# Kernel optimization log

Hardware: AMD Instinct MI355X
Metric: run time of the kernel (lower is better)

## Reference

```python
import jax, jax.numpy as jnp
import numpy as np

EPS = 1e-20
BETA = 0.25


def setup_inputs() -> dict:
    key = jax.random.key(0)
    k1, k2, k3 = jax.random.split(key, 3)
    B, N, D = 8192, 8192, 512
    x = jax.random.normal(k1, (B, D), dtype=jnp.float32)
    codebook = jax.random.normal(k2, (N, D), dtype=jnp.float32)
    u = jax.random.uniform(k3, (B, N), dtype=jnp.float32)
    return {"x": x, "codebook": codebook, "u": u}


def reference(x, codebook, u):
    # gumbel noise from uniform samples (matches sample_gumble)
    g = -jnp.log(-jnp.log(u + EPS) + EPS)  # [B, N]
    dist = (jnp.sum(x * x, axis=1, keepdims=True)
            - 2.0 * (x @ codebook.T)
            + jnp.sum(codebook * codebook, axis=1)[None, :])
    # topk(k=1) over -dist == argmin over dist
    ind = jnp.argmin(dist, axis=1)  # [B]
    # gumbel_softmax with temperature=1.0 on logits=-dist
    weights = jax.nn.softmax(-dist + g, axis=-1)  # [B, N]
    quantized = weights @ codebook  # [B, D]
    sg = jax.lax.stop_gradient
    loss = (BETA * jnp.sum((x - sg(quantized)) ** 2, axis=-1)
            + jnp.sum((sg(x) - quantized) ** 2, axis=-1))  # [B]
    return quantized, ind, loss
```

## Files before the change

kernel.cpp:

```cpp
#include <hip/hip_runtime.h>
#include <math.h>

constexpr int B = 8192, N = 8192, D = 512;
constexpr float EPSF = 1e-20f;
constexpr float SKIP   = 20.0f;
constexpr float GMAX   = 17.0f;
constexpr float DELTAF = 1.0f;
constexpr float DELTA  = 0.05f;
constexpr int CAP  = 96;
constexpr int DCAP = 48;

typedef short bf16x8 __attribute__((ext_vector_type(8)));
typedef float f32x4 __attribute__((ext_vector_type(4)));

__device__ inline unsigned short f2bf(float f) {
    unsigned x = __float_as_uint(f);
    unsigned r = x + 0x7FFFu + ((x >> 16) & 1u);
    return (unsigned short)(r >> 16);
}
__device__ inline float bf2f(unsigned short h) {
    return __uint_as_float(((unsigned)h) << 16);
}
__device__ inline unsigned fmap(float f) {
    unsigned b = __float_as_uint(f);
    return b ^ ((unsigned)((int)b >> 31) | 0x80000000u);
}
__device__ inline float funmap(unsigned u) {
    unsigned b = u ^ ((~(unsigned)((int)u >> 31)) | 0x80000000u);
    return __uint_as_float(b);
}
__device__ inline void gload16(const void* g, void* l) {
    __builtin_amdgcn_global_load_lds(
        (const __attribute__((address_space(1))) void*)g,
        (__attribute__((address_space(3))) void*)l, 16, 0, 0);
}


__global__ __launch_bounds__(256) void vq_prep(const float* __restrict__ x,
        const float* __restrict__ cb, unsigned short* __restrict__ ch,
        float* __restrict__ cnorm, float* __restrict__ xnorm,
        int* __restrict__ counts, int* __restrict__ dcounts) {
    int w = threadIdx.x >> 6, lane = threadIdx.x & 63;
    int gid = blockIdx.x * 256 + threadIdx.x;
    if (gid < 2 * B) { counts[gid] = 0; dcounts[gid] = 0; }
    int v = blockIdx.x * 4 + w;
    if (v < N) {
        const float4* s4 = reinterpret_cast<const float4*>(cb + (size_t)v * D) + lane * 2;
        float4 a = s4[0], c = s4[1];
        float vals[8] = {a.x, a.y, a.z, a.w, c.x, c.y, c.z, c.w};
        float ns = 0.f;
        unsigned short hb[8];
        #pragma unroll
        for (int e = 0; e < 8; ++e) {
            float vv = vals[e];
            ns += vv * vv;
            hb[e] = f2bf(vv);
        }
        #pragma unroll
        for (int off = 1; off < 64; off <<= 1) ns += __shfl_xor(ns, off);
        if (lane == 0) cnorm[v] = ns;
        *reinterpret_cast<bf16x8*>(ch + (size_t)v * D + lane * 8) = *reinterpret_cast<bf16x8*>(hb);
    } else {
        int b = v - N;
        const float4* s4 = reinterpret_cast<const float4*>(x + (size_t)b * D) + lane * 2;
        float4 a = s4[0], c = s4[1];
        float ns = a.x*a.x + a.y*a.y + a.z*a.z + a.w*a.w
                 + c.x*c.x + c.y*c.y + c.z*c.z + c.w*c.w;
        #pragma unroll
        for (int off = 1; off < 64; off <<= 1) ns += __shfl_xor(ns, off);
        if (lane == 0) xnorm[b] = ns;
    }
}

constexpr int OFF_B0 = 0;
constexpr int OFF_RM = 65536;
constexpr int OFF_R1 = 65792;
constexpr int OFF_CT = 66048;
constexpr int OFF_DC = 66304;
constexpr int OFF_P1 = 66560;
constexpr int OFF_P2 = 67072;
constexpr int OFF_PI = 67584;
constexpr int SMEM_BYTES = 68096;

__global__ __launch_bounds__(512, 2) void vq_mfma(
        const float* __restrict__ x, const unsigned short* __restrict__ ch,
        const float* __restrict__ cnorm, const float* __restrict__ xnorm,
        const float* __restrict__ u,
        int2* __restrict__ lists, int* __restrict__ counts,
        int* __restrict__ dlists, int* __restrict__ dcounts,
        float* __restrict__ m1h, float* __restrict__ m2h, int* __restrict__ i1h) {

    __shared__ __align__(16) unsigned char smem[SMEM_BYTES];

    const int tid = threadIdx.x, w = tid >> 6, lane = tid & 63;
    const int wm = w >> 1, wn = w & 1, l15 = lane & 15, g = lane >> 4;
    const int rg = blockIdx.x >> 1, half = blockIdx.x & 1;
    const int rbase = rg * 64, nb0 = half * 4096;

    bf16x8 ah[16];
    {
        const float* xp = x + (size_t)(rbase + wm * 16 + l15) * D + g * 8;
        #pragma unroll
        for (int ks = 0; ks < 16; ++ks) {
            const float4* p = reinterpret_cast<const float4*>(xp + ks * 32);
            float4 v0 = p[0], v1 = p[1];
            float vv[8] = {v0.x, v0.y, v0.z, v0.w, v1.x, v1.y, v1.z, v1.w};
            unsigned short hh[8];
            #pragma unroll
            for (int e = 0; e < 8; ++e) hh[e] = f2bf(vv[e]);
            ah[ks] = *reinterpret_cast<bf16x8*>(hh);
        }
    }
    float xn_r[4];
    #pragma unroll
    for (int r = 0; r < 4; ++r) xn_r[r] = xnorm[rbase + wm * 16 + g * 4 + r];

    if (tid < 64) {
        *(unsigned*)(smem + OFF_RM + tid * 4) = fmap(-INFINITY);
        *(unsigned*)(smem + OFF_R1 + tid * 4) = fmap(INFINITY);
        *(int*)(smem + OFF_CT + tid * 4) = 0;
        *(int*)(smem + OFF_DC + tid * 4) = 0;
    }

    float d1[4], d2[4], lmax[4]; int i1[4];
    #pragma unroll
    for (int r = 0; r < 4; ++r) {
        d1[r] = INFINITY; d2[r] = INFINITY; lmax[r] = -INFINITY; i1[r] = 0;
    }

    auto stage = [&](int nbn) {
        #pragma unroll
        for (int j = 0; j < 8; ++j) {
            const int row = w * 8 + j;
            const int c = (lane ^ j) * 8;
            gload16(ch + (size_t)(nbn + row) * D + c,
                    smem + OFF_B0 + row * 1024);
        }
    };

    stage(nb0);
    __syncthreads();

    const int colA = wn * 32 + l15;
    const int xr = colA & 7;
    const unsigned char* baseH = smem + OFF_B0 + colA * 1024;
    const float* ubase = u + (size_t)(rbase + wm * 16 + g * 4) * N + wn * 32 + l15;

    float dsv_prev[2][4], ur_prev[2][4];

    auto epi_fast = [&](float (&dsvX)[2][4], float (&urX)[2][4], int nbX) {
        float rmF[4], r1F[4];
        #pragma unroll
        for (int r = 0; r < 4; ++r) {
            int rl = wm * 16 + g * 4 + r;
            rmF[r] = funmap(*(const unsigned*)(smem + OFF_RM + rl * 4));
            r1F[r] = funmap(*(const unsigned*)(smem + OFF_R1 + rl * 4));
        }
        #pragma unroll
        for (int f = 0; f < 2; ++f)
            #pragma unroll
            for (int r = 0; r < 4; ++r) {
                const int rl = wm * 16 + g * 4 + r;
                const int grow = rbase + rl;
                float ds = dsvX[f][r];
                int cidx = nbX + wn * 32 + f * 16 + l15;
                if (ds < d1[r]) { d2[r] = d1[r]; d1[r] = ds; i1[r] = cidx; }
                else if (ds < d2[r]) d2[r] = ds;
                bool need = (ds < fminf(r1F[r], d1[r]) + DELTAF)
                         || (ds < GMAX + SKIP - fmaxf(rmF[r], lmax[r]));
                if (__any(need)) {
                    float gn = -__logf(-__logf(urX[f][r] + EPSF) + EPSF);
                    float lg = gn - ds;
                    lmax[r] = fmaxf(lmax[r], lg);
                    if (ds < fminf(r1F[r], d1[r]) + DELTAF) {
                        int slot = atomicAdd((int*)(smem + OFF_DC + rl * 4), 1);
                        if (slot < DCAP) dlists[(size_t)(half * B + grow) * DCAP + slot] = cidx;
                    }
                    if (ds < r1F[r]) atomicMin((unsigned*)(smem + OFF_R1 + rl * 4), fmap(ds));
                    if (lg > fmaxf(rmF[r], lmax[r]) - SKIP) {
                        int slot = atomicAdd((int*)(smem + OFF_CT + rl * 4), 1);
                        if (slot < CAP)
                            lists[(size_t)(half * B + grow) * CAP + slot] =
                                make_int2(__float_as_int(lg), cidx);
                    }
                    if (lg > rmF[r]) atomicMax((unsigned*)(smem + OFF_RM + rl * 4), fmap(lg));
                }
            }
    };

    #pragma unroll 1
    for (int t = 0; t < 64; ++t) {
        const int nb = nb0 + t * 64;
        float ur[2][4];
        #pragma unroll
        for (int f = 0; f < 2; ++f)
            #pragma unroll
            for (int r = 0; r < 4; ++r)
                ur[f][r] = ubase[(size_t)r * N + f * 16 + nb];
        float cn0 = cnorm[nb + wn * 32 + l15];
        float cn1 = cnorm[nb + wn * 32 + 16 + l15];

        f32x4 a0e = {0.f,0.f,0.f,0.f}, a0o = {0.f,0.f,0.f,0.f};
        f32x4 a1e = {0.f,0.f,0.f,0.f}, a1o = {0.f,0.f,0.f,0.f};
        #pragma unroll
        for (int ks = 0; ks < 16; ++ks) {
            const int pos = (((ks * 4 + g) ^ xr) << 4);
            bf16x8 b0 = *reinterpret_cast<const bf16x8*>(baseH + pos);
            bf16x8 b1 = *reinterpret_cast<const bf16x8*>(baseH + 16 * 1024 + pos);
            if (ks & 1) {
                a0o = __builtin_amdgcn_mfma_f32_16x16x32_bf16(ah[ks], b0, a0o, 0, 0, 0);
                a1o = __builtin_amdgcn_mfma_f32_16x16x32_bf16(ah[ks], b1, a1o, 0, 0, 0);
            } else {
                a0e = __builtin_amdgcn_mfma_f32_16x16x32_bf16(ah[ks], b0, a0e, 0, 0, 0);
                a1e = __builtin_amdgcn_mfma_f32_16x16x32_bf16(ah[ks], b1, a1e, 0, 0, 0);
            }
        }
        __syncthreads();

        if (t < 63) stage(nb + 64);

        if (t >= 2) epi_fast(dsv_prev, ur_prev, nb - 64);

        float dsv[2][4];
        #pragma unroll
        for (int f = 0; f < 2; ++f)
            #pragma unroll
            for (int r = 0; r < 4; ++r) {
                float S = f ? (a1e[r] + a1o[r]) : (a0e[r] + a0o[r]);
                dsv[f][r] = xn_r[r] - 2.f * S + (f ? cn1 : cn0);
            }

        if (t == 0) {
            float lgv0[2][4];
            #pragma unroll
            for (int f = 0; f < 2; ++f)
                #pragma unroll
                for (int r = 0; r < 4; ++r) {
                    float ds = dsv[f][r];
                    float gn = -__logf(-__logf(ur[f][r] + EPSF) + EPSF);
                    lgv0[f][r] = gn - ds;
                    int cidx = nb + wn * 32 + f * 16 + l15;
                    if (ds < d1[r]) { d2[r] = d1[r]; d1[r] = ds; i1[r] = cidx; }
                    else if (ds < d2[r]) d2[r] = ds;
                    lmax[r] = fmaxf(lmax[r], lgv0[f][r]);
                }
            #pragma unroll
            for (int r = 0; r < 4; ++r) {
                float mx = lmax[r], mn = d1[r];
                #pragma unroll
                for (int off = 1; off < 16; off <<= 1) {
                    mx = fmaxf(mx, __shfl_xor(mx, off));
                    mn = fminf(mn, __shfl_xor(mn, off));
                }
                if (l15 == 0) {
                    int rl = wm * 16 + g * 4 + r;
                    atomicMax((unsigned*)(smem + OFF_RM + rl * 4), fmap(mx));
                    atomicMin((unsigned*)(smem + OFF_R1 + rl * 4), fmap(mn));
                }
            }
            __syncthreads();
            float rmF[4], r1F[4];
            #pragma unroll
            for (int r = 0; r < 4; ++r) {
                int rl = wm * 16 + g * 4 + r;
                rmF[r] = funmap(*(const unsigned*)(smem + OFF_RM + rl * 4));
                r1F[r] = funmap(*(const unsigned*)(smem + OFF_R1 + rl * 4));
            }
            #pragma unroll
            for (int f = 0; f < 2; ++f)
                #pragma unroll
                for (int r = 0; r < 4; ++r) {
                    const int rl = wm * 16 + g * 4 + r;
                    const int grow = rbase + rl;
                    float ds = dsv[f][r], lg = lgv0[f][r];
                    int cidx = nb + wn * 32 + f * 16 + l15;
                    if (ds < fminf(r1F[r], d1[r]) + DELTAF) {
                        int slot = atomicAdd((int*)(smem + OFF_DC + rl * 4), 1);
                        if (slot < DCAP) dlists[(size_t)(half * B + grow) * DCAP + slot] = cidx;
                    }
                    if (ds < r1F[r]) atomicMin((unsigned*)(smem + OFF_R1 + rl * 4), fmap(ds));
                    if (lg > fmaxf(rmF[r], lmax[r]) - SKIP) {
                        int slot = atomicAdd((int*)(smem + OFF_CT + rl * 4), 1);
                        if (slot < CAP)
                            lists[(size_t)(half * B + grow) * CAP + slot] =
                                make_int2(__float_as_int(lg), cidx);
                    }
                    if (lg > rmF[r]) atomicMax((unsigned*)(smem + OFF_RM + rl * 4), fmap(lg));
                }
        } else {
            #pragma unroll
            for (int f = 0; f < 2; ++f)
                #pragma unroll
                for (int r = 0; r < 4; ++r) {
                    dsv_prev[f][r] = dsv[f][r];
                    ur_prev[f][r] = ur[f][r];
                }
        }
        __syncthreads();
    }
    epi_fast(dsv_prev, ur_prev, nb0 + 63 * 64);

    #pragma unroll
    for (int r = 0; r < 4; ++r) {
        float D1 = d1[r], D2v = d2[r]; int I1 = i1[r];
        #pragma unroll
        for (int off = 1; off < 16; off <<= 1) {
            float o1 = __shfl_xor(D1, off), o2 = __shfl_xor(D2v, off);
            int oi = __shfl_xor(I1, off);
            if (o1 < D1 || (o1 == D1 && oi < I1)) { D2v = fminf(D1, o2); D1 = o1; I1 = oi; }
            else D2v = fminf(o1, D2v);
        }
        if (l15 == 0) {
            int rl = wm * 16 + g * 4 + r;
            *(float*)(smem + OFF_P1 + (wn * 64 + rl) * 4) = D1;
            *(float*)(smem + OFF_P2 + (wn * 64 + rl) * 4) = D2v;
            *(int*)(smem + OFF_PI + (wn * 64 + rl) * 4) = I1;
        }
    }
    __syncthreads();
    if (tid < 64) {
        float a1 = *(float*)(smem + OFF_P1 + tid * 4), a2 = *(float*)(smem + OFF_P2 + tid * 4);
        int ai = *(int*)(smem + OFF_PI + tid * 4);
        float b1 = *(float*)(smem + OFF_P1 + (64 + tid) * 4), b2 = *(float*)(smem + OFF_P2 + (64 + tid) * 4);
        int bi = *(int*)(smem + OFF_PI + (64 + tid) * 4);
        float m1, m2; int mi;
        if (b1 < a1 || (b1 == a1 && bi < ai)) { m1 = b1; mi = bi; m2 = fminf(a1, b2); }
        else                                  { m1 = a1; mi = ai; m2 = fminf(b1, a2); }
        int hrow = half * B + rbase + tid;
        m1h[hrow] = m1; m2h[hrow] = m2; i1h[hrow] = mi;
        counts[hrow] = *(int*)(smem + OFF_CT + tid * 4);
        dcounts[hrow] = *(int*)(smem + OFF_DC + tid * 4);
    }
}

__global__ __launch_bounds__(256) void vq_finalize(
        const float* __restrict__ cb, const float* __restrict__ x,
        const int2* __restrict__ lists, const int* __restrict__ counts,
        float* __restrict__ m1h, float* __restrict__ m2h, int* __restrict__ i1h,
        float* __restrict__ out_q, float* __restrict__ out_loss) {
    __shared__ int2 ebuf[4][2 * CAP];
    int w = threadIdx.x >> 6, lane = threadIdx.x & 63;
    int row = blockIdx.x * 4 + w;
    int n0 = counts[row];      if (n0 > CAP) n0 = CAP;
    int n1 = counts[B + row];  if (n1 > CAP) n1 = CAP;
    int n = n0 + n1;
    for (int e = lane; e < n0; e += 64) ebuf[w][e] = lists[(size_t)row * CAP + e];
    for (int e = lane; e < n1; e += 64) ebuf[w][n0 + e] = lists[(size_t)(B + row) * CAP + e];
    __syncthreads();
    float m = -INFINITY;
    for (int e = lane; e < n; e += 64) m = fmaxf(m, __int_as_float(ebuf[w][e].x));
    #pragma unroll
    for (int off = 1; off < 64; off <<= 1) m = fmaxf(m, __shfl_xor(m, off));
    float denom = 0.f;
    for (int e = lane; e < n; e += 64) denom += __expf(__int_as_float(ebuf[w][e].x) - m);
    #pragma unroll
    for (int off = 1; off < 64; off <<= 1) denom += __shfl_xor(denom, off);
    float q[8] = {0.f, 0.f, 0.f, 0.f, 0.f, 0.f, 0.f, 0.f};
    for (int e = 0; e < n; ++e) {
        int2 ent = ebuf[w][e];
        float wgt = __expf(__int_as_float(ent.x) - m);
        if (wgt < 1e-9f) continue;
        const float4* c4 = reinterpret_cast<const float4*>(cb + (size_t)ent.y * D + lane * 8);
        float4 c0 = c4[0], c1 = c4[1];
        q[0] += wgt * c0.x; q[1] += wgt * c0.y; q[2] += wgt * c0.z; q[3] += wgt * c0.w;
        q[4] += wgt * c1.x; q[5] += wgt * c1.y; q[6] += wgt * c1.z; q[7] += wgt * c1.w;
    }
    float inv = 1.f / denom;
    const float4* x4 = reinterpret_cast<const float4*>(x + (size_t)row * D + lane * 8);
    float4 xa = x4[0], xb = x4[1];
    float xs[8] = {xa.x, xa.y, xa.z, xa.w, xb.x, xb.y, xb.z, xb.w};
    float ls = 0.f;
    #pragma unroll
    for (int k = 0; k < 8; ++k) {
        q[k] *= inv;
        float dlt = xs[k] - q[k];
        ls += dlt * dlt;
    }
    float4 q0 = {q[0], q[1], q[2], q[3]}, q1 = {q[4], q[5], q[6], q[7]};
    float4* o = reinterpret_cast<float4*>(out_q + (size_t)row * D + lane * 8);
    o[0] = q0; o[1] = q1;
    #pragma unroll
    for (int off = 1; off < 64; off <<= 1) ls += __shfl_xor(ls, off);
    if (lane == 0) {
        out_loss[row] = 1.25f * ls;
        float a1 = m1h[row], a2 = m2h[row]; int ai = i1h[row];
        float b1 = m1h[B + row], b2 = m2h[B + row]; int bi = i1h[B + row];
        float mm1, mm2; int mi;
        if (b1 < a1 || (b1 == a1 && bi < ai)) { mm1 = b1; mi = bi; mm2 = fminf(a1, b2); }
        else                                  { mm1 = a1; mi = ai; mm2 = fminf(b1, a2); }
        m1h[row] = mm1; m2h[row] = mm2; i1h[row] = mi;
    }
}

__global__ __launch_bounds__(256) void vq_row_full(
        const float* __restrict__ x, const float* __restrict__ cb,
        const float* __restrict__ cnorm, const float* __restrict__ u,
        const int* __restrict__ counts,
        float* __restrict__ out_q, float* __restrict__ out_loss) {
    int row = blockIdx.x;
    if (counts[row] <= CAP && counts[B + row] <= CAP) return;
    int tid = threadIdx.x, wv_ = tid >> 6, lane = tid & 63;
    __shared__ float xs[D];
    __shared__ float red[4];
    __shared__ float wts[256]; __shared__ int ids[256]; __shared__ int nc;
    for (int i = tid; i < D; i += 256) xs[i] = x[(size_t)row * D + i];
    if (tid == 0) nc = 0;
    __syncthreads();
    float xn = 0.f;
    for (int i = tid; i < D; i += 256) xn += xs[i] * xs[i];
    #pragma unroll
    for (int off = 1; off < 64; off <<= 1) xn += __shfl_xor(xn, off);
    if (lane == 0) red[wv_] = xn;
    __syncthreads();
    xn = red[0] + red[1] + red[2] + red[3];
    __syncthreads();
    float m = -INFINITY;
    for (int n = tid; n < N; n += 256) {
        float dot = 0.f;
        const float* c = cb + (size_t)n * D;
        for (int d = 0; d < D; ++d) dot = fmaf(xs[d], c[d], dot);
        float lg = -__logf(-__logf(u[(size_t)row * N + n] + EPSF) + EPSF)
                 - (xn - 2.f * dot + cnorm[n]);
        m = fmaxf(m, lg);
    }
    #pragma unroll
    for (int off = 1; off < 64; off <<= 1) m = fmaxf(m, __shfl_xor(m, off));
    if (lane == 0) red[wv_] = m;
    __syncthreads();
    m = fmaxf(fmaxf(red[0], red[1]), fmaxf(red[2], red[3]));
    __syncthreads();
    float denom = 0.f;
    for (int n = tid; n < N; n += 256) {
        float dot = 0.f;
        const float* c = cb + (size_t)n * D;
        for (int d = 0; d < D; ++d) dot = fmaf(xs[d], c[d], dot);
        float lg = -__logf(-__logf(u[(size_t)row * N + n] + EPSF) + EPSF)
                 - (xn - 2.f * dot + cnorm[n]);
        float wv2 = __expf(lg - m);
        denom += wv2;
        if (wv2 > 1e-8f) {
            int s = atomicAdd(&nc, 1);
            if (s < 256) { wts[s] = wv2; ids[s] = n; }
        }
    }
    #pragma unroll
    for (int off = 1; off < 64; off <<= 1) denom += __shfl_xor(denom, off);
    if (lane == 0) red[wv_] = denom;
    __syncthreads();
    denom = red[0] + red[1] + red[2] + red[3];
    int ncl = nc < 256 ? nc : 256;
    float q0 = 0.f, q1 = 0.f;
    for (int e = 0; e < ncl; ++e) {
        const float* c = cb + (size_t)ids[e] * D;
        q0 += wts[e] * c[tid * 2];
        q1 += wts[e] * c[tid * 2 + 1];
    }
    q0 /= denom; q1 /= denom;
    out_q[(size_t)row * D + tid * 2] = q0;
    out_q[(size_t)row * D + tid * 2 + 1] = q1;
    float dl0 = xs[tid * 2] - q0, dl1 = xs[tid * 2 + 1] - q1;
    float ls = dl0 * dl0 + dl1 * dl1;
    #pragma unroll
    for (int off = 1; off < 64; off <<= 1) ls += __shfl_xor(ls, off);
    __syncthreads();
    if (lane == 0) red[wv_] = ls;
    __syncthreads();
    if (tid == 0) out_loss[row] = 1.25f * (red[0] + red[1] + red[2] + red[3]);
}

__global__ __launch_bounds__(256) void argmin_fix2(
        const float* __restrict__ x, const float* __restrict__ cb,
        const float* __restrict__ m1h, const float* __restrict__ m2h,
        const int* __restrict__ i1h,
        const int* __restrict__ dcounts, const int* __restrict__ dlists,
        float* __restrict__ out_ind) {
    int w = threadIdx.x >> 6, lane = threadIdx.x & 63;
    int row = blockIdx.x * 4 + w;
    if (m2h[row] - m1h[row] >= DELTAF) {
        if (lane == 0) out_ind[row] = (float)i1h[row];
        return;
    }
    const float4* x4 = reinterpret_cast<const float4*>(x + (size_t)row * D) + lane * 2;
    float4 xa = x4[0], xb = x4[1];
    double xd[8] = {(double)xa.x, (double)xa.y, (double)xa.z, (double)xa.w,
                    (double)xb.x, (double)xb.y, (double)xb.z, (double)xb.w};
    double bestv = 1e300; int besti = 0x7fffffff;

    auto evalCode = [&](int n) {
        const float4* c4 = reinterpret_cast<const float4*>(cb + (size_t)n * D) + lane * 2;
        float4 ca = c4[0], cbv = c4[1];
        double cd[8] = {(double)ca.x, (double)ca.y, (double)ca.z, (double)ca.w,
                        (double)cbv.x, (double)cbv.y, (double)cbv.z, (double)cbv.w};
        double s = 0.0;
        #pragma unroll
        for (int k = 0; k < 8; ++k) {
            double dlt = xd[k] - cd[k];
            s = fma(dlt, dlt, s);
        }
        #pragma unroll
        for (int off = 1; off < 64; off <<= 1) s += __shfl_xor(s, off);
        if (s < bestv || (s == bestv && n < besti)) { bestv = s; besti = n; }
    };

    int n0 = dcounts[row], n1 = dcounts[B + row];
    if (n0 <= DCAP && n1 <= DCAP) {
        evalCode(i1h[row]);
        for (int e = 0; e < n0; ++e) evalCode(dlists[(size_t)row * DCAP + e]);
        for (int e = 0; e < n1; ++e) evalCode(dlists[(size_t)(B + row) * DCAP + e]);
    } else {
        for (int n = 0; n < N; ++n) evalCode(n);
    }
    if (lane == 0) out_ind[row] = (float)besti;
}

constexpr int ROWS = 16;
constexpr int NT   = 256;
constexpr int DT   = 16;

__global__ __launch_bounds__(256) void prep_norms(const float* __restrict__ x,
                                                  const float* __restrict__ cb,
                                                  float* __restrict__ cnorm,
                                                  float* __restrict__ xnorm) {
    int wave = threadIdx.x >> 6, lane = threadIdx.x & 63;
    int v = blockIdx.x * 4 + wave;
    const float* src;
    float* dst;
    if (v < N) { src = cb + (size_t)v * D; dst = cnorm + v; }
    else       { int b = v - N; if (b >= B) return; src = x + (size_t)b * D; dst = xnorm + b; }
    const float4* s4 = reinterpret_cast<const float4*>(src) + lane * 2;
    float4 a = s4[0], c = s4[1];
    float s = a.x*a.x + a.y*a.y + a.z*a.z + a.w*a.w
            + c.x*c.x + c.y*c.y + c.z*c.z + c.w*c.w;
    #pragma unroll
    for (int off = 1; off < 64; off <<= 1) s += __shfl_xor(s, off);
    if (lane == 0) *dst = s;
}

__global__ __launch_bounds__(256) void vq_main(const float* __restrict__ x,
        const float* __restrict__ cb, const float* __restrict__ u,
        const float* __restrict__ cnorm, const float* __restrict__ xnorm,
        float* __restrict__ out_q, float* __restrict__ out_loss,
        float* __restrict__ m1w, float* __restrict__ m2w, int* __restrict__ i1w) {

    __shared__ float xs[ROWS][D];
    __shared__ float ct[DT][NT];

    const int tid  = threadIdx.x;
    const int wave = tid >> 6, lane = tid & 63;
    const int rbase = blockIdx.x * ROWS;
    const int wrow  = rbase + wave * 4;

    for (int i = tid; i < ROWS * (D / 4); i += 256)
        reinterpret_cast<float4*>(xs)[i] =
            reinterpret_cast<const float4*>(x + (size_t)rbase * D)[i];
    __syncthreads();

    float xn[4];
    #pragma unroll
    for (int r = 0; r < 4; ++r) xn[r] = xnorm[wrow + r];

    float m[4], denom[4], acc[4][8];
    float am1[4], am2[4]; int ai1[4];
    #pragma unroll
    for (int r = 0; r < 4; ++r) {
        m[r] = -INFINITY; denom[r] = 0.f;
        am1[r] = INFINITY; am2[r] = INFINITY; ai1[r] = 0;
        #pragma unroll
        for (int k = 0; k < 8; ++k) acc[r][k] = 0.f;
    }

    for (int nb = 0; nb < N; nb += NT) {
        float S[4][4];
        #pragma unroll
        for (int r = 0; r < 4; ++r)
            #pragma unroll
            for (int j = 0; j < 4; ++j) S[r][j] = 0.f;

        for (int db = 0; db < D; db += DT) {
            __syncthreads();
            {
                const float4* src = reinterpret_cast<const float4*>(
                        cb + (size_t)(nb + tid) * D + db);
                float4 a0 = src[0], a1 = src[1], a2 = src[2], a3 = src[3];
                ct[ 0][tid]=a0.x; ct[ 1][tid]=a0.y; ct[ 2][tid]=a0.z; ct[ 3][tid]=a0.w;
                ct[ 4][tid]=a1.x; ct[ 5][tid]=a1.y; ct[ 6][tid]=a1.z; ct[ 7][tid]=a1.w;
                ct[ 8][tid]=a2.x; ct[ 9][tid]=a2.y; ct[10][tid]=a2.z; ct[11][tid]=a2.w;
                ct[12][tid]=a3.x; ct[13][tid]=a3.y; ct[14][tid]=a3.z; ct[15][tid]=a3.w;
            }
            __syncthreads();
            #pragma unroll
            for (int dq = 0; dq < DT / 4; ++dq) {
                float creg[4][4];
                #pragma unroll
                for (int k = 0; k < 4; ++k) {
                    float4 cv = *reinterpret_cast<const float4*>(&ct[dq*4 + k][4*lane]);
                    creg[k][0]=cv.x; creg[k][1]=cv.y; creg[k][2]=cv.z; creg[k][3]=cv.w;
                }
                #pragma unroll
                for (int r = 0; r < 4; ++r) {
                    float4 xv = *reinterpret_cast<const float4*>(&xs[wave*4 + r][db + dq*4]);
                    float xr[4] = {xv.x, xv.y, xv.z, xv.w};
                    #pragma unroll
                    for (int k = 0; k < 4; ++k)
                        #pragma unroll
                        for (int j = 0; j < 4; ++j)
                            S[r][j] = fmaf(xr[k], creg[k][j], S[r][j]);
                }
            }
        }

        float4 cn4 = *reinterpret_cast<const float4*>(&cnorm[nb + 4*lane]);
        float cn[4] = {cn4.x, cn4.y, cn4.z, cn4.w};

        float logit[4][4], dist[4][4];
        #pragma unroll
        for (int r = 0; r < 4; ++r) {
            float4 u4 = *reinterpret_cast<const float4*>(
                    &u[(size_t)(wrow + r) * N + nb + 4*lane]);
            float uu[4] = {u4.x, u4.y, u4.z, u4.w};
            #pragma unroll
            for (int j = 0; j < 4; ++j) {
                float ds = xn[r] - 2.f * S[r][j] + cn[j];
                float gg  = -logf(-logf(uu[j] + EPSF) + EPSF);
                dist[r][j]  = ds;
                logit[r][j] = gg - ds;
            }
        }

        #pragma unroll
        for (int r = 0; r < 4; ++r) {
            float l1 = INFINITY, l2 = INFINITY; int li = 0;
            #pragma unroll
            for (int j = 0; j < 4; ++j) {
                float dv = dist[r][j]; int idx = nb + 4*lane + j;
                if (dv < l1)      { l2 = l1; l1 = dv; li = idx; }
                else if (dv < l2) { l2 = dv; }
            }
            #pragma unroll
            for (int off = 1; off < 64; off <<= 1) {
                float o1 = __shfl_xor(l1, off), o2 = __shfl_xor(l2, off);
                int   oi = __shfl_xor(li, off);
                if (o1 < l1 || (o1 == l1 && oi < li)) { l2 = fminf(l1, o2); l1 = o1; li = oi; }
                else                                  { l2 = fminf(o1, l2); }
            }
            if (l1 < am1[r] || (l1 == am1[r] && li < ai1[r])) {
                am2[r] = fminf(am1[r], l2); am1[r] = l1; ai1[r] = li;
            } else {
                am2[r] = fminf(am2[r], l1);
            }

            float lm = fmaxf(fmaxf(logit[r][0], logit[r][1]),
                             fmaxf(logit[r][2], logit[r][3]));
            #pragma unroll
            for (int off = 1; off < 64; off <<= 1) lm = fmaxf(lm, __shfl_xor(lm, off));
            if (lm > m[r]) {
                float s = expf(m[r] - lm);
                denom[r] *= s;
                #pragma unroll
                for (int k = 0; k < 8; ++k) acc[r][k] *= s;
                m[r] = lm;
            }

            float wv[4];
            #pragma unroll
            for (int j = 0; j < 4; ++j) {
                float e = logit[r][j] - m[r];
                bool act = e > -SKIP;
                wv[j] = act ? expf(e) : 0.f;
                denom[r] += wv[j];
            }
            #pragma unroll
            for (int j = 0; j < 4; ++j) {
                unsigned long long mk = __ballot(wv[j] > 0.f);
                while (mk) {
                    int L = __ffsll((unsigned long long)mk) - 1;
                    mk &= mk - 1;
                    float wb = __shfl(wv[j], L);
                    int nstar = nb + 4*L + j;
                    const float4* crow = reinterpret_cast<const float4*>(
                            cb + (size_t)nstar * D + 8*lane);
                    float4 c0 = crow[0], c1 = crow[1];
                    acc[r][0] = fmaf(wb, c0.x, acc[r][0]);
                    acc[r][1] = fmaf(wb, c0.y, acc[r][1]);
                    acc[r][2] = fmaf(wb, c0.z, acc[r][2]);
                    acc[r][3] = fmaf(wb, c0.w, acc[r][3]);
                    acc[r][4] = fmaf(wb, c1.x, acc[r][4]);
                    acc[r][5] = fmaf(wb, c1.y, acc[r][5]);
                    acc[r][6] = fmaf(wb, c1.z, acc[r][6]);
                    acc[r][7] = fmaf(wb, c1.w, acc[r][7]);
                }
            }
        }
    }

    #pragma unroll
    for (int r = 0; r < 4; ++r) {
        float dn = denom[r];
        #pragma unroll
        for (int off = 1; off < 64; off <<= 1) dn += __shfl_xor(dn, off);
        float inv = 1.f / dn;
        int row = wrow + r;
        float q[8]; float ls = 0.f;
        #pragma unroll
        for (int k = 0; k < 8; ++k) {
            q[k] = acc[r][k] * inv;
            float dlt = xs[wave*4 + r][8*lane + k] - q[k];
            ls += dlt * dlt;
        }
        float4 q0 = {q[0], q[1], q[2], q[3]}, q1 = {q[4], q[5], q[6], q[7]};
        float4* o = reinterpret_cast<float4*>(out_q + (size_t)row * D + 8*lane);
        o[0] = q0; o[1] = q1;
        #pragma unroll
        for (int off = 1; off < 64; off <<= 1) ls += __shfl_xor(ls, off);
        if (lane == 0) {
            out_loss[row] = 1.25f * ls;
            m1w[row] = am1[r]; m2w[row] = am2[r]; i1w[row] = ai1[r];
        }
    }
}

__global__ __launch_bounds__(256) void argmin_fix(const float* __restrict__ x,
        const float* __restrict__ cb, const float* __restrict__ m1w,
        const float* __restrict__ m2w, const int* __restrict__ i1w,
        float* __restrict__ out_ind) {
    int b = blockIdx.x, tid = threadIdx.x;
    if (m2w[b] - m1w[b] >= DELTA) {
        if (tid == 0) out_ind[b] = (float)i1w[b];
        return;
    }
    __shared__ double xsd[D];
    for (int i = tid; i < D; i += 256) xsd[i] = (double)x[(size_t)b * D + i];
    __syncthreads();
    double xn = 0.0;
    for (int d = 0; d < D; ++d) xn += xsd[d] * xsd[d];

    double bestv = 1e300; int besti = N;
    for (int n = tid; n < N; n += 256) {
        const float* c = cb + (size_t)n * D;
        double d0 = 0.0, d1v = 0.0, c0 = 0.0, c1v = 0.0;
        for (int d = 0; d < D; d += 2) {
            double ca = (double)c[d], cbv = (double)c[d + 1];
            d0 += xsd[d] * ca;  c0 += ca * ca;
            d1v += xsd[d + 1] * cbv; c1v += cbv * cbv;
        }
        double dv = xn - 2.0 * (d0 + d1v) + (c0 + c1v);
        if (dv < bestv || (dv == bestv && n < besti)) { bestv = dv; besti = n; }
    }
    __shared__ double rv[256]; __shared__ int ri[256];
    rv[tid] = bestv; ri[tid] = besti;
    __syncthreads();
    for (int s = 128; s > 0; s >>= 1) {
        if (tid < s) {
            if (rv[tid+s] < rv[tid] || (rv[tid+s] == rv[tid] && ri[tid+s] < ri[tid])) {
                rv[tid] = rv[tid+s]; ri[tid] = ri[tid+s];
            }
        }
        __syncthreads();
    }
    if (tid == 0) out_ind[b] = (float)ri[0];
}

extern "C" void kernel_launch(void* const* d_in, const int* in_sizes, int n_in,
                              void* d_out, int out_size, void* d_ws, size_t ws_size,
                              hipStream_t stream) {
    const float* x  = (const float*)d_in[0];
    const float* cb = (const float*)d_in[1];
    const float* u  = (const float*)d_in[2];
    float* out      = (float*)d_out;
    float* out_q    = out;
    float* out_ind  = out + (size_t)B * D;
    float* out_loss = out_ind + B;

    const size_t O_CH = 0;
    const size_t O_CN = O_CH + (size_t)N * D * 2;
    const size_t O_XN = O_CN + (size_t)N * 4;
    const size_t O_M1 = O_XN + (size_t)B * 4;
    const size_t O_M2 = O_M1 + (size_t)2 * B * 4;
    const size_t O_I1 = O_M2 + (size_t)2 * B * 4;
    const size_t O_CT = O_I1 + (size_t)2 * B * 4;
    const size_t O_DC = O_CT + (size_t)2 * B * 4;
    const size_t O_LS = O_DC + (size_t)2 * B * 4;
    const size_t O_DL = O_LS + (size_t)2 * B * CAP * 8;
    const size_t NEED = O_DL + (size_t)2 * B * DCAP * 4;

    if (ws_size >= NEED) {
        char* w8 = (char*)d_ws;
        unsigned short* ch = (unsigned short*)(w8 + O_CH);
        float* cnorm = (float*)(w8 + O_CN);
        float* xnorm = (float*)(w8 + O_XN);
        float* m1h   = (float*)(w8 + O_M1);
        float* m2h   = (float*)(w8 + O_M2);
        int*   i1h   = (int*)(w8 + O_I1);
        int*   counts= (int*)(w8 + O_CT);
        int*   dcounts=(int*)(w8 + O_DC);
        int2*  lists = (int2*)(w8 + O_LS);
        int*   dlists= (int*)(w8 + O_DL);

        hipLaunchKernelGGL(vq_prep, dim3((N + B) / 4), dim3(256), 0, stream,
                           x, cb, ch, cnorm, xnorm, counts, dcounts);
        hipLaunchKernelGGL(vq_mfma, dim3(256), dim3(512), 0, stream,
                           x, ch, cnorm, xnorm, u, lists, counts,
                           dlists, dcounts, m1h, m2h, i1h);
        hipLaunchKernelGGL(vq_finalize, dim3(B / 4), dim3(256), 0, stream,
                           cb, x, lists, counts, m1h, m2h, i1h, out_q, out_loss);
        hipLaunchKernelGGL(vq_row_full, dim3(B), dim3(256), 0, stream,
                           x, cb, cnorm, u, counts, out_q, out_loss);
        hipLaunchKernelGGL(argmin_fix2, dim3(B / 4), dim3(256), 0, stream,
                           x, cb, m1h, m2h, i1h, dcounts, dlists, out_ind);
    } else {
        float* ws    = (float*)d_ws;
        float* cnorm = ws;
        float* xnorm = ws + N;
        float* m1w   = xnorm + B;
        float* m2w   = m1w + B;
        int*   i1w   = (int*)(m2w + B);

        hipLaunchKernelGGL(prep_norms, dim3((N + B) / 4), dim3(256), 0, stream,
                           x, cb, cnorm, xnorm);
        hipLaunchKernelGGL(vq_main, dim3(B / ROWS), dim3(256), 0, stream,
                           x, cb, u, cnorm, xnorm, out_q, out_loss, m1w, m2w, i1w);
        hipLaunchKernelGGL(argmin_fix, dim3(B), dim3(256), 0, stream,
                           x, cb, m1w, m2w, i1w, out_ind);
    }
}
```

Measured before the change: 285.4 us.

## Remap MFMA warp tiling to 2x4 with shared B fragment across two row tiles

Changes the wave layout from 4x2 (16 rows x 32 cols per wave) to 2x4 (32 rows x 16 cols per wave), so each wave holds two A row fragments and reuses one LDS B fragment for both MFMAs. This halves LDS reads of the codebook tile per MFMA, and the cross-wave argmin merge now combines four column partials instead of two. Holding twice the A registers raises register pressure, so launch bounds drop to one block per CU-slot, which may reduce occupancy and latency hiding.

```diff
diff --git a/kernel.cpp b/kernel.cpp
--- a/kernel.cpp
+++ b/kernel.cpp
@@ -78,11 +78,11 @@
 constexpr int OFF_CT = 66048;
 constexpr int OFF_DC = 66304;
 constexpr int OFF_P1 = 66560;
-constexpr int OFF_P2 = 67072;
-constexpr int OFF_PI = 67584;
-constexpr int SMEM_BYTES = 68096;
-
-__global__ __launch_bounds__(512, 2) void vq_mfma(
+constexpr int OFF_P2 = 67584;
+constexpr int OFF_PI = 68608;
+constexpr int SMEM_BYTES = 69632;
+
+__global__ __launch_bounds__(512, 1) void vq_mfma(
         const float* __restrict__ x, const unsigned short* __restrict__ ch,
         const float* __restrict__ cnorm, const float* __restrict__ xnorm,
         const float* __restrict__ u,
@@ -93,13 +93,14 @@
     __shared__ __align__(16) unsigned char smem[SMEM_BYTES];
 
     const int tid = threadIdx.x, w = tid >> 6, lane = tid & 63;
-    const int wm = w >> 1, wn = w & 1, l15 = lane & 15, g = lane >> 4;
+    const int wm = w >> 2, wn = w & 3, l15 = lane & 15, g = lane >> 4;
     const int rg = blockIdx.x >> 1, half = blockIdx.x & 1;
     const int rbase = rg * 64, nb0 = half * 4096;
 
-    bf16x8 ah[16];
-    {
-        const float* xp = x + (size_t)(rbase + wm * 16 + l15) * D + g * 8;
+    bf16x8 ah[2][16];
+    #pragma unroll
+    for (int rf = 0; rf < 2; ++rf) {
+        const float* xp = x + (size_t)(rbase + wm * 32 + rf * 16 + l15) * D + g * 8;
         #pragma unroll
         for (int ks = 0; ks < 16; ++ks) {
             const float4* p = reinterpret_cast<const float4*>(xp + ks * 32);
@@ -108,12 +109,15 @@
             unsigned short hh[8];
             #pragma unroll
             for (int e = 0; e < 8; ++e) hh[e] = f2bf(vv[e]);
-            ah[ks] = *reinterpret_cast<bf16x8*>(hh);
-        }
-    }
-    float xn_r[4];
-    #pragma unroll
-    for (int r = 0; r < 4; ++r) xn_r[r] = xnorm[rbase + wm * 16 + g * 4 + r];
+            ah[rf][ks] = *reinterpret_cast<bf16x8*>(hh);
+        }
+    }
+    float xn_r[2][4];
+    #pragma unroll
+    for (int rf = 0; rf < 2; ++rf)
+        #pragma unroll
+        for (int r = 0; r < 4; ++r)
+            xn_r[rf][r] = xnorm[rbase + wm * 32 + rf * 16 + g * 4 + r];
 
     if (tid < 64) {
         *(unsigned*)(smem + OFF_RM + tid * 4) = fmap(-INFINITY);
@@ -122,11 +126,14 @@
         *(int*)(smem + OFF_DC + tid * 4) = 0;
     }
 
-    float d1[4], d2[4], lmax[4]; int i1[4];
-    #pragma unroll
-    for (int r = 0; r < 4; ++r) {
-        d1[r] = INFINITY; d2[r] = INFINITY; lmax[r] = -INFINITY; i1[r] = 0;
-    }
+    float d1[2][4], d2[2][4], lmax[2][4]; int i1[2][4];
+    #pragma unroll
+    for (int rf = 0; rf < 2; ++rf)
+        #pragma unroll
+        for (int r = 0; r < 4; ++r) {
+            d1[rf][r] = INFINITY; d2[rf][r] = INFINITY;
+            lmax[rf][r] = -INFINITY; i1[rf][r] = 0;
+        }
 
     auto stage = [&](int nbn) {
         #pragma unroll
@@ -141,49 +148,51 @@
     stage(nb0);
     __syncthreads();
 
-    const int colA = wn * 32 + l15;
+    const int colA = wn * 16 + l15;
     const int xr = colA & 7;
     const unsigned char* baseH = smem + OFF_B0 + colA * 1024;
-    const float* ubase = u + (size_t)(rbase + wm * 16 + g * 4) * N + wn * 32 + l15;
+    const float* ubase = u + (size_t)(rbase + wm * 32 + g * 4) * N + wn * 16 + l15;
 
     float dsv_prev[2][4], ur_prev[2][4];
 
     auto epi_fast = [&](float (&dsvX)[2][4], float (&urX)[2][4], int nbX) {
-        float rmF[4], r1F[4];
-        #pragma unroll
-        for (int r = 0; r < 4; ++r) {
-            int rl = wm * 16 + g * 4 + r;
-            rmF[r] = funmap(*(const unsigned*)(smem + OFF_RM + rl * 4));
-            r1F[r] = funmap(*(const unsigned*)(smem + OFF_R1 + rl * 4));
-        }
-        #pragma unroll
-        for (int f = 0; f < 2; ++f)
+        float rmF[2][4], r1F[2][4];
+        #pragma unroll
+        for (int rf = 0; rf < 2; ++rf)
             #pragma unroll
             for (int r = 0; r < 4; ++r) {
-                const int rl = wm * 16 + g * 4 + r;
+                int rl = wm * 32 + rf * 16 + g * 4 + r;
+                rmF[rf][r] = funmap(*(const unsigned*)(smem + OFF_RM + rl * 4));
+                r1F[rf][r] = funmap(*(const unsigned*)(smem + OFF_R1 + rl * 4));
+            }
+        const int cidx = nbX + wn * 16 + l15;
+        #pragma unroll
+        for (int rf = 0; rf < 2; ++rf)
+            #pragma unroll
+            for (int r = 0; r < 4; ++r) {
+                const int rl = wm * 32 + rf * 16 + g * 4 + r;
                 const int grow = rbase + rl;
-                float ds = dsvX[f][r];
-                int cidx = nbX + wn * 32 + f * 16 + l15;
-                if (ds < d1[r]) { d2[r] = d1[r]; d1[r] = ds; i1[r] = cidx; }
-                else if (ds < d2[r]) d2[r] = ds;
-                bool need = (ds < fminf(r1F[r], d1[r]) + DELTAF)
-                         || (ds < GMAX + SKIP - fmaxf(rmF[r], lmax[r]));
+                float ds = dsvX[rf][r];
+                if (ds < d1[rf][r]) { d2[rf][r] = d1[rf][r]; d1[rf][r] = ds; i1[rf][r] = cidx; }
+                else if (ds < d2[rf][r]) d2[rf][r] = ds;
+                bool need = (ds < fminf(r1F[rf][r], d1[rf][r]) + DELTAF)
+                         || (ds < GMAX + SKIP - fmaxf(rmF[rf][r], lmax[rf][r]));
                 if (__any(need)) {
-                    float gn = -__logf(-__logf(urX[f][r] + EPSF) + EPSF);
+                    float gn = -__logf(-__logf(urX[rf][r] + EPSF) + EPSF);
                     float lg = gn - ds;
-                    lmax[r] = fmaxf(lmax[r], lg);
-                    if (ds < fminf(r1F[r], d1[r]) + DELTAF) {
+                    lmax[rf][r] = fmaxf(lmax[rf][r], lg);
+                    if (ds < fminf(r1F[rf][r], d1[rf][r]) + DELTAF) {
                         int slot = atomicAdd((int*)(smem + OFF_DC + rl * 4), 1);
                         if (slot < DCAP) dlists[(size_t)(half * B + grow) * DCAP + slot] = cidx;
                     }
-                    if (ds < r1F[r]) atomicMin((unsigned*)(smem + OFF_R1 + rl * 4), fmap(ds));
-                    if (lg > fmaxf(rmF[r], lmax[r]) - SKIP) {
+                    if (ds < r1F[rf][r]) atomicMin((unsigned*)(smem + OFF_R1 + rl * 4), fmap(ds));
+                    if (lg > fmaxf(rmF[rf][r], lmax[rf][r]) - SKIP) {
                         int slot = atomicAdd((int*)(smem + OFF_CT + rl * 4), 1);
                         if (slot < CAP)
                             lists[(size_t)(half * B + grow) * CAP + slot] =
                                 make_int2(__float_as_int(lg), cidx);
                     }
-                    if (lg > rmF[r]) atomicMax((unsigned*)(smem + OFF_RM + rl * 4), fmap(lg));
+                    if (lg > rmF[rf][r]) atomicMax((unsigned*)(smem + OFF_RM + rl * 4), fmap(lg));
                 }
             }
     };
@@ -193,12 +202,11 @@
         const int nb = nb0 + t * 64;
         float ur[2][4];
         #pragma unroll
-        for (int f = 0; f < 2; ++f)
+        for (int rf = 0; rf < 2; ++rf)
             #pragma unroll
             for (int r = 0; r < 4; ++r)
-                ur[f][r] = ubase[(size_t)r * N + f * 16 + nb];
-        float cn0 = cnorm[nb + wn * 32 + l15];
-        float cn1 = cnorm[nb + wn * 32 + 16 + l15];
+                ur[rf][r] = ubase[(size_t)(rf * 16 + r) * N + nb];
+        float cn0 = cnorm[nb + wn * 16 + l15];
 
         f32x4 a0e = {0.f,0.f,0.f,0.f}, a0o = {0.f,0.f,0.f,0.f};
         f32x4 a1e = {0.f,0.f,0.f,0.f}, a1o = {0.f,0.f,0.f,0.f};
@@ -206,13 +214,12 @@
         for (int ks = 0; ks < 16; ++ks) {
             const int pos = (((ks * 4 + g) ^ xr) << 4);
             bf16x8 b0 = *reinterpret_cast<const bf16x8*>(baseH + pos);
-            bf16x8 b1 = *reinterpret_cast<const bf16x8*>(baseH + 16 * 1024 + pos);
             if (ks & 1) {
-                a0o = __builtin_amdgcn_mfma_f32_16x16x32_bf16(ah[ks], b0, a0o, 0, 0, 0);
-                a1o = __builtin_amdgcn_mfma_f32_16x16x32_bf16(ah[ks], b1, a1o, 0, 0, 0);
+                a0o = __builtin_amdgcn_mfma_f32_16x16x32_bf16(ah[0][ks], b0, a0o, 0, 0, 0);
+                a1o = __builtin_amdgcn_mfma_f32_16x16x32_bf16(ah[1][ks], b0, a1o, 0, 0, 0);
             } else {
-                a0e = __builtin_amdgcn_mfma_f32_16x16x32_bf16(ah[ks], b0, a0e, 0, 0, 0);
-                a1e = __builtin_amdgcn_mfma_f32_16x16x32_bf16(ah[ks], b1, a1e, 0, 0, 0);
+                a0e = __builtin_amdgcn_mfma_f32_16x16x32_bf16(ah[0][ks], b0, a0e, 0, 0, 0);
+                a1e = __builtin_amdgcn_mfma_f32_16x16x32_bf16(ah[1][ks], b0, a1e, 0, 0, 0);
             }
         }
         __syncthreads();
@@ -223,77 +230,73 @@
 
         float dsv[2][4];
         #pragma unroll
-        for (int f = 0; f < 2; ++f)
+        for (int rf = 0; rf < 2; ++rf)
             #pragma unroll
             for (int r = 0; r < 4; ++r) {
-                float S = f ? (a1e[r] + a1o[r]) : (a0e[r] + a0o[r]);
-                dsv[f][r] = xn_r[r] - 2.f * S + (f ? cn1 : cn0);
+                float S = rf ? (a1e[r] + a1o[r]) : (a0e[r] + a0o[r]);
+                dsv[rf][r] = xn_r[rf][r] - 2.f * S + cn0;
             }
 
         if (t == 0) {
             float lgv0[2][4];
-            #pragma unroll
-            for (int f = 0; f < 2; ++f)
+            const int cidx0 = nb + wn * 16 + l15;
+            #pragma unroll
+            for (int rf = 0; rf < 2; ++rf)
                 #pragma unroll
                 for (int r = 0; r < 4; ++r) {
-                    float ds = dsv[f][r];
-                    float gn = -__logf(-__logf(ur[f][r] + EPSF) + EPSF);
-                    lgv0[f][r] = gn - ds;
-                    int cidx = nb + wn * 32 + f * 16 + l15;
-                    if (ds < d1[r]) { d2[r] = d1[r]; d1[r] = ds; i1[r] = cidx; }
-                    else if (ds < d2[r]) d2[r] = ds;
-                    lmax[r] = fmaxf(lmax[r], lgv0[f][r]);
+                    float ds = dsv[rf][r];
+                    float gn = -__logf(-__logf(ur[rf][r] + EPSF) + EPSF);
+                    lgv0[rf][r] = gn - ds;
+                    if (ds < d1[rf][r]) { d2[rf][r] = d1[rf][r]; d1[rf][r] = ds; i1[rf][r] = cidx0; }
+                    else if (ds < d2[rf][r]) d2[rf][r] = ds;
+                    lmax[rf][r] = fmaxf(lmax[rf][r], lgv0[rf][r]);
                 }
             #pragma unroll
-            for (int r = 0; r < 4; ++r) {
-                float mx = lmax[r], mn = d1[r];
-                #pragma unroll
-                for (int off = 1; off < 16; off <<= 1) {
-                    mx = fmaxf(mx, __shfl_xor(mx, off));
-                    mn = fminf(mn, __shfl_xor(mn, off));
-                }
-                if (l15 == 0) {
-                    int rl = wm * 16 + g * 4 + r;
-                    atomicMax((unsigned*)(smem + OFF_RM + rl * 4), fmap(mx));
-                    atomicMin((unsigned*)(smem + OFF_R1 + rl * 4), fmap(mn));
-                }
-            }
-            __syncthreads();
-            float rmF[4], r1F[4];
-            #pragma unroll
-            for (int r = 0; r < 4; ++r) {
-                int rl = wm * 16 + g * 4 + r;
-                rmF[r] = funmap(*(const unsigned*)(smem + OFF_RM + rl * 4));
-                r1F[r] = funmap(*(const unsigned*)(smem + OFF_R1 + rl * 4));
-            }
-            #pragma unroll
-            for (int f = 0; f < 2; ++f)
+            for (int rf = 0; rf < 2; ++rf)
                 #pragma unroll
                 for (int r = 0; r < 4; ++r) {
-                    const int rl = wm * 16 + g * 4 + r;
+                    float mx = lmax[rf][r], mn = d1[rf][r];
+                    #pragma unroll
+                    for (int off = 1; off < 16; off <<= 1) {
+                        mx = fmaxf(mx, __shfl_xor(mx, off));
+                        mn = fminf(mn, __shfl_xor(mn, off));
+                    }
+                    if (l15 == 0) {
+                        int rl = wm * 32 + rf * 16 + g * 4 + r;
+                        atomicMax((unsigned*)(smem + OFF_RM + rl * 4), fmap(mx));
+                        atomicMin((unsigned*)(smem + OFF_R1 + rl * 4), fmap(mn));
+                    }
+                }
+            __syncthreads();
+            #pragma unroll
+            for (int rf = 0; rf < 2; ++rf)
+                #pragma unroll
+                for (int r = 0; r < 4; ++r) {
+                    const int rl = wm * 32 + rf * 16 + g * 4 + r;
                     const int grow = rbase + rl;
-                    float ds = dsv[f][r], lg = lgv0[f][r];
-                    int cidx = nb + wn * 32 + f * 16 + l15;
-                    if (ds < fminf(r1F[r], d1[r]) + DELTAF) {
+                    float rmF = funmap(*(const unsigned*)(smem + OFF_RM + rl * 4));
+                    float r1F = funmap(*(const unsigned*)(smem + OFF_R1 + rl * 4));
+                    float ds = dsv[rf][r], lg = lgv0[rf][r];
+                    if (ds < fminf(r1F, d1[rf][r]) + DELTAF) {
                         int slot = atomicAdd((int*)(smem + OFF_DC + rl * 4), 1);
-                        if (slot < DCAP) dlists[(size_t)(half * B + grow) * DCAP + slot] = cidx;
+                        if (slot < DCAP) dlists[(size_t)(half * B + grow) * DCAP + slot] = cidx0;
                     }
-                    if (ds < r1F[r]) atomicMin((unsigned*)(smem + OFF_R1 + rl * 4), fmap(ds));
-                    if (lg > fmaxf(rmF[r], lmax[r]) - SKIP) {
+                    if (ds < r1F) atomicMin((unsigned*)(smem + OFF_R1 + rl * 4), fmap(ds));
+                    if (lg > fmaxf(rmF, lmax[rf][r]) - SKIP) {
                         int slot = atomicAdd((int*)(smem + OFF_CT + rl * 4), 1);
                         if (slot < CAP)
                             lists[(size_t)(half * B + grow) * CAP + slot] =
-                                make_int2(__float_as_int(lg), cidx);
+                                make_int2(__float_as_int(lg), cidx0);
                     }
-                    if (lg > rmF[r]) atomicMax((unsigned*)(smem + OFF_RM + rl * 4), fmap(lg));
+                    if (lg > rmF) atomicMax((unsigned*)(smem + OFF_RM + rl * 4), fmap(lg));
                 }
         } else {
             #pragma unroll
-            for (int f = 0; f < 2; ++f)
+            for (int rf = 0; rf < 2; ++rf)
                 #pragma unroll
                 for (int r = 0; r < 4; ++r) {
-                    dsv_prev[f][r] = dsv[f][r];
-                    ur_prev[f][r] = ur[f][r];
+                    dsv_prev[rf][r] = dsv[rf][r];
+                    ur_prev[rf][r] = ur[rf][r];
                 }
         }
         __syncthreads();
@@ -301,33 +304,38 @@
     epi_fast(dsv_prev, ur_prev, nb0 + 63 * 64);
 
     #pragma unroll
-    for (int r = 0; r < 4; ++r) {
-        float D1 = d1[r], D2v = d2[r]; int I1 = i1[r];
-        #pragma unroll
-        for (int off = 1; off < 16; off <<= 1) {
-            float o1 = __shfl_xor(D1, off), o2 = __shfl_xor(D2v, off);
-            int oi = __shfl_xor(I1, off);
-            if (o1 < D1 || (o1 == D1 && oi < I1)) { D2v = fminf(D1, o2); D1 = o1; I1 = oi; }
-            else D2v = fminf(o1, D2v);
-        }
-        if (l15 == 0) {
-            int rl = wm * 16 + g * 4 + r;
-            *(float*)(smem + OFF_P1 + (wn * 64 + rl) * 4) = D1;
-            *(float*)(smem + OFF_P2 + (wn * 64 + rl) * 4) = D2v;
-            *(int*)(smem + OFF_PI + (wn * 64 + rl) * 4) = I1;
-        }
-    }
+    for (int rf = 0; rf < 2; ++rf)
+        #pragma unroll
+        for (int r = 0; r < 4; ++r) {
+            float D1 = d1[rf][r], D2v = d2[rf][r]; int I1 = i1[rf][r];
+            #pragma unroll
+            for (int off = 1; off < 16; off <<= 1) {
+                float o1 = __shfl_xor(D1, off), o2 = __shfl_xor(D2v, off);
+                int oi = __shfl_xor(I1, off);
+                if (o1 < D1 || (o1 == D1 && oi < I1)) { D2v = fminf(D1, o2); D1 = o1; I1 = oi; }
+                else D2v = fminf(o1, D2v);
+            }
+            if (l15 == 0) {
+                int rl = wm * 32 + rf * 16 + g * 4 + r;
+                *(float*)(smem + OFF_P1 + (wn * 64 + rl) * 4) = D1;
+                *(float*)(smem + OFF_P2 + (wn * 64 + rl) * 4) = D2v;
+                *(int*)(smem + OFF_PI + (wn * 64 + rl) * 4) = I1;
+            }
+        }
     __syncthreads();
     if (tid < 64) {
         float a1 = *(float*)(smem + OFF_P1 + tid * 4), a2 = *(float*)(smem + OFF_P2 + tid * 4);
         int ai = *(int*)(smem + OFF_PI + tid * 4);
-        float b1 = *(float*)(smem + OFF_P1 + (64 + tid) * 4), b2 = *(float*)(smem + OFF_P2 + (64 + tid) * 4);
-        int bi = *(int*)(smem + OFF_PI + (64 + tid) * 4);
-        float m1, m2; int mi;
-        if (b1 < a1 || (b1 == a1 && bi < ai)) { m1 = b1; mi = bi; m2 = fminf(a1, b2); }
-        else                                  { m1 = a1; mi = ai; m2 = fminf(b1, a2); }
+        #pragma unroll
+        for (int wv = 1; wv < 4; ++wv) {
+            float b1 = *(float*)(smem + OFF_P1 + (wv * 64 + tid) * 4);
+            float b2 = *(float*)(smem + OFF_P2 + (wv * 64 + tid) * 4);
+            int bi = *(int*)(smem + OFF_PI + (wv * 64 + tid) * 4);
+            if (b1 < a1 || (b1 == a1 && bi < ai)) { a2 = fminf(a1, b2); a1 = b1; ai = bi; }
+            else a2 = fminf(b1, a2);
+        }
         int hrow = half * B + rbase + tid;
-        m1h[hrow] = m1; m2h[hrow] = m2; i1h[hrow] = mi;
+        m1h[hrow] = a1; m2h[hrow] = a2; i1h[hrow] = ai;
         counts[hrow] = *(int*)(smem + OFF_CT + tid * 4);
         dcounts[hrow] = *(int*)(smem + OFF_DC + tid * 4);
     }
```

Result: slower. 711.5 us (+149.3%).
